# Performance work log

Measured on AMD Instinct MI355X. Metric: run time of the kernel, lower is better.

The kernel has to match this reference:

```python
import jax, jax.numpy as jnp
import numpy as np

N, E, D, H, L = 20000, 320000, 128, 8, 3
C = D // H  # per-head channels = 16


def setup_inputs() -> dict:
    key = jax.random.key(0)
    ks = jax.random.split(key, 20)
    s = 1.0 / np.sqrt(D)
    inp = {
        "x": jax.random.normal(ks[0], (N, D), dtype=jnp.float32),
        "edge_index": jax.random.randint(ks[1], (2, E), 0, N, dtype=jnp.int64),
        "Wq": jax.random.normal(ks[2], (L, D, D), dtype=jnp.float32) * s,
        "bq": jnp.zeros((L, D), dtype=jnp.float32),
        "Wk": jax.random.normal(ks[3], (L, D, D), dtype=jnp.float32) * s,
        "bk": jnp.zeros((L, D), dtype=jnp.float32),
        "Wv": jax.random.normal(ks[4], (L, D, D), dtype=jnp.float32) * s,
        "bv": jnp.zeros((L, D), dtype=jnp.float32),
        "Wskip": jax.random.normal(ks[5], (L, D, D), dtype=jnp.float32) * s,
        "bskip": jnp.zeros((L, D), dtype=jnp.float32),
        "Wbeta": jax.random.normal(ks[6], (L, 3 * D, 1), dtype=jnp.float32) * (1.0 / np.sqrt(3 * D)),
        "ln_g": jnp.ones((L, D), dtype=jnp.float32),
        "ln_b": jnp.zeros((L, D), dtype=jnp.float32),
        "Wout": jax.random.normal(ks[7], (D, D), dtype=jnp.float32) * s,
        "bout": jnp.zeros((D,), dtype=jnp.float32),
    }
    return inp


def _layer_norm(x, g, b, eps=1e-5):
    mu = jnp.mean(x, axis=-1, keepdims=True)
    var = jnp.mean(jnp.square(x - mu), axis=-1, keepdims=True)
    return (x - mu) * jax.lax.rsqrt(var + eps) * g + b


def _transformer_conv(x, src, dst, Wq, bq, Wk, bk, Wv, bv, Wskip, bskip, Wbeta):
    # project q/k/v: [N, D] -> [N, H, C]
    q = (x @ Wq + bq).reshape(N, H, C)
    k = (x @ Wk + bk).reshape(N, H, C)
    v = (x @ Wv + bv).reshape(N, H, C)
    # per-edge attention logits: [E, H]
    alpha = jnp.sum(q[dst] * k[src], axis=-1) / np.sqrt(C)
    # scatter-softmax over edges grouped by dst node
    m = jax.ops.segment_max(alpha, dst, num_segments=N)  # [N, H]
    m = jnp.where(jnp.isfinite(m), m, 0.0)
    ea = jnp.exp(alpha - m[dst])
    denom = jax.ops.segment_sum(ea, dst, num_segments=N)  # [N, H]
    attn = ea / (denom[dst] + 1e-16)  # [E, H]
    # weighted message aggregation: [N, H, C] -> [N, D]
    out = jax.ops.segment_sum(attn[:, :, None] * v[src], dst, num_segments=N)
    out = out.reshape(N, D)
    # beta-gated skip connection (beta=True, root_weight=True)
    x_r = x @ Wskip + bskip
    beta = jax.nn.sigmoid(jnp.concatenate([out, x_r, out - x_r], axis=-1) @ Wbeta)  # [N, 1]
    return beta * x_r + (1.0 - beta) * out


def reference(x, edge_index, Wq, bq, Wk, bk, Wv, bv, Wskip, bskip, Wbeta, ln_g, ln_b, Wout, bout):
    src, dst = edge_index[0], edge_index[1]
    for i in range(L):
        residual = x
        x = _transformer_conv(x, src, dst, Wq[i], bq[i], Wk[i], bk[i], Wv[i], bv[i],
                              Wskip[i], bskip[i], Wbeta[i])
        x = jax.nn.relu(x)  # dropout is identity in eval mode
        x = _layer_norm(x + residual, ln_g[i], ln_b[i])
    return x @ Wout + bout
```

## Files before the change

### kernel.cpp

```cpp
#include <hip/hip_runtime.h>

#define N_NODES 20000
#define N_EDGES 320000
#define DIM 128
#define NLAYER 3
#define SCAN_BLK 1024
#define N_SCAN_BLKS ((N_NODES + SCAN_BLK - 1) / SCAN_BLK)
#define LDS_STRIDE 136

typedef __attribute__((ext_vector_type(8))) short short8;
typedef __attribute__((ext_vector_type(4))) float f32x4;

__device__ inline ushort f2bf(float f) {
  uint u = __float_as_uint(f);
  uint r = (u + 0x7fffu + ((u >> 16) & 1u)) >> 16;
  return (ushort)r;
}
__device__ inline float bf2f(ushort u) { return __uint_as_float(((uint)u) << 16); }


__global__ void zero_ints_kernel(int* __restrict__ p, int n) {
  int i = blockIdx.x * 256 + threadIdx.x;
  if (i < n) p[i] = 0;
}

__global__ void count_deg_kernel(const int* __restrict__ ei, int* __restrict__ deg) {
  int e = blockIdx.x * 256 + threadIdx.x;
  if (e < N_EDGES) atomicAdd(&deg[ei[N_EDGES + e]], 1);
}

__global__ __launch_bounds__(SCAN_BLK) void scan1_kernel(const int* __restrict__ deg,
                                                         int* __restrict__ rowptr,
                                                         int* __restrict__ blksum) {
  __shared__ int wsum[16];
  int t = threadIdx.x, lane = t & 63, w = t >> 6;
  int i = blockIdx.x * SCAN_BLK + t;
  int val = (i < N_NODES) ? deg[i] : 0;
  int s = val;
  #pragma unroll
  for (int off = 1; off < 64; off <<= 1) {
    int u = __shfl_up(s, off);
    if (lane >= off) s += u;
  }
  if (lane == 63) wsum[w] = s;
  __syncthreads();
  if (t < 16) {
    int wv = wsum[t];
    int ss = wv;
    #pragma unroll
    for (int off = 1; off < 16; off <<= 1) {
      int u = __shfl_up(ss, off);
      if (t >= off) ss += u;
    }
    wsum[t] = ss - wv;
  }
  __syncthreads();
  int excl = wsum[w] + s - val;
  if (i < N_NODES) rowptr[i] = excl;
  if (t == SCAN_BLK - 1) blksum[blockIdx.x] = excl + val;
}

__global__ void scan2_kernel(int* __restrict__ blksum, int* __restrict__ rowptr) {
  int t = threadIdx.x;
  int val = (t < N_SCAN_BLKS) ? blksum[t] : 0;
  int s = val;
  #pragma unroll
  for (int off = 1; off < 64; off <<= 1) {
    int u = __shfl_up(s, off);
    if (t >= off) s += u;
  }
  if (t < N_SCAN_BLKS) blksum[t] = s - val;
  if (t == 63) rowptr[N_NODES] = s;
}

__global__ __launch_bounds__(SCAN_BLK) void scan3_kernel(int* __restrict__ rowptr,
                                                         const int* __restrict__ blksum,
                                                         int* __restrict__ degc) {
  int i = blockIdx.x * SCAN_BLK + threadIdx.x;
  if (i < N_NODES) {
    rowptr[i] += blksum[blockIdx.x];
    degc[i] = 0;
  }
}

__global__ void scatter_kernel(const int* __restrict__ ei, const int* __restrict__ rowptr,
                               int* __restrict__ cursor, int* __restrict__ csr_src) {
  int e = blockIdx.x * 256 + threadIdx.x;
  if (e < N_EDGES) {
    int d = ei[N_EDGES + e];
    int s = ei[e];
    int pos = atomicAdd(&cursor[d], 1);
    csr_src[rowptr[d] + pos] = s;
  }
}


__global__ void cast_x_kernel(const float* __restrict__ x, ushort* __restrict__ xb, int n4) {
  int i = blockIdx.x * 256 + threadIdx.x;
  if (i < n4) {
    float4 f = ((const float4*)x)[i];
    ushort4 o;
    o.x = f2bf(f.x); o.y = f2bf(f.y); o.z = f2bf(f.z); o.w = f2bf(f.w);
    ((ushort4*)xb)[i] = o;
  }
}

__global__ void cast_w_kernel(const float* __restrict__ Wq, const float* __restrict__ Wk,
                              const float* __restrict__ Wv, const float* __restrict__ Ws,
                              const float* __restrict__ Wo, ushort* __restrict__ wt) {
  int z = blockIdx.z;
  const float* src;
  if (z < 12) {
    int l = z >> 2, j = z & 3;
    src = (j == 0 ? Wq : j == 1 ? Wk : j == 2 ? Wv : Ws) + (size_t)l * DIM * DIM;
  } else {
    src = Wo;
  }
  __shared__ float tile[32][33];
  int tx = threadIdx.x, ty = threadIdx.y;
  int k0 = blockIdx.x * 32, n0 = blockIdx.y * 32;
  #pragma unroll
  for (int i = 0; i < 32; i += 8)
    tile[ty + i][tx] = src[(size_t)(k0 + ty + i) * DIM + n0 + tx];
  __syncthreads();
  ushort* dst = wt + (size_t)z * DIM * DIM;
  #pragma unroll
  for (int i = 0; i < 32; i += 8)
    dst[(size_t)(n0 + ty + i) * DIM + k0 + tx] = f2bf(tile[tx][ty + i]);
}

template <int OUT_BF16>
__global__ __launch_bounds__(256) void gemm_mfma_kernel(
    const ushort* __restrict__ X, const ushort* __restrict__ WT,
    const float* __restrict__ B0, const float* __restrict__ B1,
    const float* __restrict__ B2, const float* __restrict__ B3,
    void* __restrict__ O0, void* __restrict__ O1, void* __restrict__ O2,
    void* __restrict__ O3) {
  __shared__ ushort As[128 * LDS_STRIDE];
  int mat = blockIdx.y;
  const ushort* Wt = WT + (size_t)mat * DIM * DIM;
  const float* bias;
  void* O;
  switch (mat) {
    case 0: bias = B0; O = O0; break;
    case 1: bias = B1; O = O1; break;
    case 2: bias = B2; O = O2; break;
    default: bias = B3; O = O3; break;
  }
  int t = threadIdx.x;
  int wid = t >> 6, lane = t & 63;
  int row0 = blockIdx.x * 128;
  int wr = wid >> 1, wc = wid & 1;
  int lr = lane & 15;
  int kc8 = (lane >> 4) * 8;

  {
    int rowi = t >> 4;
    int col = (t & 15) * 8;
    #pragma unroll
    for (int pass = 0; pass < 8; ++pass) {
      int row = pass * 16 + rowi;
      int gr = min(row0 + row, N_NODES - 1);
      short8 val = *(const short8*)(X + (size_t)gr * DIM + col);
      *(short8*)(As + row * LDS_STRIDE + col) = val;
    }
  }
  __syncthreads();

  f32x4 acc[4][4];
  #pragma unroll
  for (int i = 0; i < 4; ++i)
    #pragma unroll
    for (int j = 0; j < 4; ++j) acc[i][j] = (f32x4){0.f, 0.f, 0.f, 0.f};

  #pragma unroll
  for (int ks = 0; ks < 4; ++ks) {
    short8 b[4];
    #pragma unroll
    for (int cf = 0; cf < 4; ++cf) {
      int c = wc * 64 + cf * 16 + lr;
      b[cf] = *(const short8*)(Wt + (size_t)c * DIM + ks * 32 + kc8);
    }
    #pragma unroll
    for (int rf = 0; rf < 4; ++rf) {
      int r = wr * 64 + rf * 16 + lr;
      short8 a = *(const short8*)(As + r * LDS_STRIDE + ks * 32 + kc8);
      #pragma unroll
      for (int cf = 0; cf < 4; ++cf)
        acc[rf][cf] = __builtin_amdgcn_mfma_f32_16x16x32_bf16(a, b[cf], acc[rf][cf], 0, 0, 0);
    }
  }

  #pragma unroll
  for (int cf = 0; cf < 4; ++cf) {
    int c = wc * 64 + cf * 16 + lr;
    float bv = bias[c];
    #pragma unroll
    for (int rf = 0; rf < 4; ++rf) {
      #pragma unroll
      for (int reg = 0; reg < 4; ++reg) {
        int r = row0 + wr * 64 + rf * 16 + (lane >> 4) * 4 + reg;
        if (r < N_NODES) {
          float val = acc[rf][cf][reg] + bv;
          if (OUT_BF16)
            ((ushort*)O)[(size_t)r * DIM + c] = f2bf(val);
          else
            ((float*)O)[(size_t)r * DIM + c] = val;
        }
      }
    }
  }
}

__global__ __launch_bounds__(64) void attn_fused_kernel(
    const ushort* __restrict__ q, const ushort* __restrict__ k, const ushort* __restrict__ v,
    const ushort* __restrict__ xr, const float* __restrict__ xres,
    const int* __restrict__ rowptr, const int* __restrict__ csr_src,
    const float* __restrict__ wbeta, const float* __restrict__ lng,
    const float* __restrict__ lnb, float* __restrict__ xnext,
    ushort* __restrict__ xnextb) {
  __shared__ float lds_s[8][20];
  int n = blockIdx.x;
  int lane = threadIdx.x;
  int h = lane & 7, e = lane >> 3;

  const ushort* qrow = q + (size_t)n * DIM + h * 16;
  short8 q0 = *(const short8*)qrow;
  short8 q1 = *(const short8*)(qrow + 8);
  float qf[16];
  #pragma unroll
  for (int i = 0; i < 8; ++i) {
    qf[i] = bf2f((ushort)q0[i]);
    qf[8 + i] = bf2f((ushort)q1[i]);
  }

  int s0 = rowptr[n];
  int deg = rowptr[n + 1] - s0;
  float acc[16];
  #pragma unroll
  for (int i = 0; i < 16; ++i) acc[i] = 0.f;
  float dsum = 0.f;

  for (int base = 0; base < deg; base += 8) {
    int idx = base + e;
    bool valid = idx < deg;
    int src = csr_src[s0 + min(idx, deg - 1)];
    const ushort* kr = k + (size_t)src * DIM + h * 16;
    const ushort* vr = v + (size_t)src * DIM + h * 16;
    short8 ka = *(const short8*)kr;
    short8 kb2 = *(const short8*)(kr + 8);
    short8 va = *(const short8*)vr;
    short8 vb2 = *(const short8*)(vr + 8);
    float p0 = 0.f, p1 = 0.f;
    #pragma unroll
    for (int i = 0; i < 8; ++i) {
      p0 = fmaf(qf[i], bf2f((ushort)ka[i]), p0);
      p1 = fmaf(qf[8 + i], bf2f((ushort)kb2[i]), p1);
    }
    float ea = __expf((p0 + p1) * 0.25f);
    ea = valid ? ea : 0.f;
    dsum += ea;
    #pragma unroll
    for (int i = 0; i < 8; ++i) {
      acc[i] = fmaf(ea, bf2f((ushort)va[i]), acc[i]);
      acc[8 + i] = fmaf(ea, bf2f((ushort)vb2[i]), acc[8 + i]);
    }
  }

  #pragma unroll
  for (int off = 8; off <= 32; off <<= 1) {
    dsum += __shfl_xor(dsum, off);
    #pragma unroll
    for (int i = 0; i < 16; ++i) acc[i] += __shfl_xor(acc[i], off);
  }
  if (lane < 8) {
    #pragma unroll
    for (int i = 0; i < 16; i += 4)
      *(float4*)&lds_s[lane][i] = make_float4(acc[i], acc[i + 1], acc[i + 2], acc[i + 3]);
    lds_s[lane][16] = dsum;
  }
  __syncthreads();

  int c0 = lane * 2;
  int hh = lane >> 3, cc = (lane & 7) * 2;
  float2 ov = *(float2*)&lds_s[hh][cc];
  float den = lds_s[hh][16];
  float inv = 1.f / (den + 1e-16f);
  float o0 = ov.x * inv, o1 = ov.y * inv;

  ushort2 xru = *(const ushort2*)(xr + (size_t)n * DIM + c0);
  float xr0 = bf2f(xru.x), xr1 = bf2f(xru.y);
  float wa0 = wbeta[c0] + wbeta[2 * DIM + c0];
  float wa1 = wbeta[c0 + 1] + wbeta[2 * DIM + c0 + 1];
  float wb0 = wbeta[DIM + c0] - wbeta[2 * DIM + c0];
  float wb1 = wbeta[DIM + c0 + 1] - wbeta[2 * DIM + c0 + 1];
  float bs = o0 * wa0 + o1 * wa1 + xr0 * wb0 + xr1 * wb1;
  #pragma unroll
  for (int off = 1; off < 64; off <<= 1) bs += __shfl_xor(bs, off);
  float beta = 1.f / (1.f + __expf(-bs));
  float y0 = fmaxf(beta * xr0 + (1.f - beta) * o0, 0.f);
  float y1 = fmaxf(beta * xr1 + (1.f - beta) * o1, 0.f);
  float2 rv = *(const float2*)(xres + (size_t)n * DIM + c0);
  y0 += rv.x;
  y1 += rv.y;
  float s = y0 + y1;
  #pragma unroll
  for (int off = 1; off < 64; off <<= 1) s += __shfl_xor(s, off);
  float mu = s * (1.f / 128.f);
  float d0 = y0 - mu, d1 = y1 - mu;
  float vs = d0 * d0 + d1 * d1;
  #pragma unroll
  for (int off = 1; off < 64; off <<= 1) vs += __shfl_xor(vs, off);
  float rstd = rsqrtf(vs * (1.f / 128.f) + 1e-5f);
  float2 g = *(const float2*)(lng + c0);
  float2 b = *(const float2*)(lnb + c0);
  float out0 = d0 * rstd * g.x + b.x;
  float out1 = d1 * rstd * g.y + b.y;
  *(float2*)(xnext + (size_t)n * DIM + c0) = make_float2(out0, out1);
  ushort2 ob;
  ob.x = f2bf(out0);
  ob.y = f2bf(out1);
  *(ushort2*)(xnextb + (size_t)n * DIM + c0) = ob;
}


extern "C" void kernel_launch(void* const* d_in, const int* in_sizes, int n_in,
                              void* d_out, int out_size, void* d_ws, size_t ws_size,
                              hipStream_t stream) {
  const float* x_in = (const float*)d_in[0];
  const int* ei = (const int*)d_in[1];
  const float* Wq = (const float*)d_in[2];
  const float* bq = (const float*)d_in[3];
  const float* Wk = (const float*)d_in[4];
  const float* bk = (const float*)d_in[5];
  const float* Wv = (const float*)d_in[6];
  const float* bv = (const float*)d_in[7];
  const float* Wsk = (const float*)d_in[8];
  const float* bsk = (const float*)d_in[9];
  const float* Wb = (const float*)d_in[10];
  const float* lng = (const float*)d_in[11];
  const float* lnb = (const float*)d_in[12];
  const float* Wout = (const float*)d_in[13];
  const float* bout = (const float*)d_in[14];
  float* out = (float*)d_out;

  char* p = (char*)d_ws;
  auto alloc = [&](size_t bytes) {
    char* r = p;
    p += (bytes + 255) & ~(size_t)255;
    return r;
  };
  const size_t NB2 = (size_t)N_NODES * DIM * 2;
  const size_t NB4 = (size_t)N_NODES * DIM * 4;
  ushort* xbb = (ushort*)alloc(NB2);
  ushort* qb = (ushort*)alloc(NB2);
  ushort* kb = (ushort*)alloc(NB2);
  ushort* vb = (ushort*)alloc(NB2);
  ushort* xrb = (ushort*)alloc(NB2);
  float* xf0 = (float*)alloc(NB4);
  float* xf1 = (float*)alloc(NB4);
  ushort* wt = (ushort*)alloc((size_t)13 * DIM * DIM * 2);
  int* rowptr = (int*)alloc((N_NODES + 1) * 4);
  int* degc = (int*)alloc(N_NODES * 4);
  int* blksum = (int*)alloc(64 * 4);
  int* csr_src = (int*)alloc(N_EDGES * 4);

  zero_ints_kernel<<<(N_NODES + 255) / 256, 256, 0, stream>>>(degc, N_NODES);
  count_deg_kernel<<<(N_EDGES + 255) / 256, 256, 0, stream>>>(ei, degc);
  scan1_kernel<<<N_SCAN_BLKS, SCAN_BLK, 0, stream>>>(degc, rowptr, blksum);
  scan2_kernel<<<1, 64, 0, stream>>>(blksum, rowptr);
  scan3_kernel<<<N_SCAN_BLKS, SCAN_BLK, 0, stream>>>(rowptr, blksum, degc);
  scatter_kernel<<<(N_EDGES + 255) / 256, 256, 0, stream>>>(ei, rowptr, degc, csr_src);

  cast_x_kernel<<<(N_NODES * DIM / 4 + 255) / 256, 256, 0, stream>>>(x_in, xbb,
                                                                     N_NODES * DIM / 4);
  cast_w_kernel<<<dim3(4, 4, 13), dim3(32, 8), 0, stream>>>(Wq, Wk, Wv, Wsk, Wout, wt);

  const int GX = (N_NODES + 127) / 128;
  const float* xres = x_in;
  float* xfbufs[NLAYER] = {xf0, xf1, xf0};
  for (int l = 0; l < NLAYER; ++l) {
    gemm_mfma_kernel<1><<<dim3(GX, 4), 256, 0, stream>>>(
        xbb, wt + (size_t)l * 4 * DIM * DIM,
        bq + (size_t)l * DIM, bk + (size_t)l * DIM, bv + (size_t)l * DIM,
        bsk + (size_t)l * DIM, qb, kb, vb, xrb);
    attn_fused_kernel<<<N_NODES, 64, 0, stream>>>(
        qb, kb, vb, xrb, xres, rowptr, csr_src,
        Wb + (size_t)l * 3 * DIM, lng + (size_t)l * DIM, lnb + (size_t)l * DIM,
        xfbufs[l], xbb);
    xres = xfbufs[l];
  }
  gemm_mfma_kernel<0><<<dim3(GX, 1), 256, 0, stream>>>(
      xbb, wt + (size_t)12 * DIM * DIM, bout, bout, bout, bout, out, out, out, out);
}
```

Measured before the change: 218.1 us.

## Interleave K/V rows, pack 4 nodes per attention block, merge prep kernels

K and V projections are written into one interleaved buffer with a 256-element row stride, so each gathered source node's K and V sit in a single contiguous 512-byte row instead of two separate arrays. The attention kernel now processes four destination nodes per 256-thread block rather than one node per 64-thread block, reducing block count and scheduling overhead. The x cast, weight transpose-cast and degree zeroing are merged into one prep kernel to cut launch count. The GEMM gains per-output strides to support the interleaved layout.

```diff
diff --git a/kernel.cpp b/kernel.cpp
--- a/kernel.cpp
+++ b/kernel.cpp
@@ -8,6 +8,11 @@
 #define N_SCAN_BLKS ((N_NODES + SCAN_BLK - 1) / SCAN_BLK)
 #define LDS_STRIDE 136
 
+#define PREP_CASTX_BLKS 2500
+#define PREP_CASTW_BLKS 208
+#define PREP_ZERO_BLKS 79
+#define PREP_TOTAL (PREP_CASTX_BLKS + PREP_CASTW_BLKS + PREP_ZERO_BLKS)
+
 typedef __attribute__((ext_vector_type(8))) short short8;
 typedef __attribute__((ext_vector_type(4))) float f32x4;
 
@@ -18,11 +23,48 @@
 }
 __device__ inline float bf2f(ushort u) { return __uint_as_float(((uint)u) << 16); }
 
-
-__global__ void zero_ints_kernel(int* __restrict__ p, int n) {
-  int i = blockIdx.x * 256 + threadIdx.x;
-  if (i < n) p[i] = 0;
-}
+__global__ __launch_bounds__(256) void prep_kernel(
+    const float* __restrict__ x, ushort* __restrict__ xb,
+    const float* __restrict__ Wq, const float* __restrict__ Wk,
+    const float* __restrict__ Wv, const float* __restrict__ Ws,
+    const float* __restrict__ Wo, ushort* __restrict__ wt,
+    int* __restrict__ degc) {
+  int b = blockIdx.x;
+  int t = threadIdx.x;
+  if (b < PREP_CASTX_BLKS) {
+    int i = b * 256 + t;
+    float4 f = ((const float4*)x)[i];
+    ushort4 o;
+    o.x = f2bf(f.x); o.y = f2bf(f.y); o.z = f2bf(f.z); o.w = f2bf(f.w);
+    ((ushort4*)xb)[i] = o;
+  } else if (b < PREP_CASTX_BLKS + PREP_CASTW_BLKS) {
+    int idx = b - PREP_CASTX_BLKS;
+    int z = idx >> 4;
+    int r = idx & 15;
+    int k0 = (r >> 2) * 32, n0 = (r & 3) * 32;
+    const float* src;
+    if (z < 12) {
+      int l = z >> 2, j = z & 3;
+      src = (j == 0 ? Wq : j == 1 ? Wk : j == 2 ? Wv : Ws) + (size_t)l * DIM * DIM;
+    } else {
+      src = Wo;
+    }
+    __shared__ float tile[32][33];
+    int tx = t & 31, ty = t >> 5;
+    #pragma unroll
+    for (int i = 0; i < 32; i += 8)
+      tile[ty + i][tx] = src[(size_t)(k0 + ty + i) * DIM + n0 + tx];
+    __syncthreads();
+    ushort* dst = wt + (size_t)z * DIM * DIM;
+    #pragma unroll
+    for (int i = 0; i < 32; i += 8)
+      dst[(size_t)(n0 + ty + i) * DIM + k0 + tx] = f2bf(tile[tx][ty + i]);
+  } else {
+    int i = (b - PREP_CASTX_BLKS - PREP_CASTW_BLKS) * 256 + t;
+    if (i < N_NODES) degc[i] = 0;
+  }
+}
+
 
 __global__ void count_deg_kernel(const int* __restrict__ ei, int* __restrict__ deg) {
   int e = blockIdx.x * 256 + threadIdx.x;
@@ -94,58 +136,24 @@
   }
 }
 
-
-__global__ void cast_x_kernel(const float* __restrict__ x, ushort* __restrict__ xb, int n4) {
-  int i = blockIdx.x * 256 + threadIdx.x;
-  if (i < n4) {
-    float4 f = ((const float4*)x)[i];
-    ushort4 o;
-    o.x = f2bf(f.x); o.y = f2bf(f.y); o.z = f2bf(f.z); o.w = f2bf(f.w);
-    ((ushort4*)xb)[i] = o;
-  }
-}
-
-__global__ void cast_w_kernel(const float* __restrict__ Wq, const float* __restrict__ Wk,
-                              const float* __restrict__ Wv, const float* __restrict__ Ws,
-                              const float* __restrict__ Wo, ushort* __restrict__ wt) {
-  int z = blockIdx.z;
-  const float* src;
-  if (z < 12) {
-    int l = z >> 2, j = z & 3;
-    src = (j == 0 ? Wq : j == 1 ? Wk : j == 2 ? Wv : Ws) + (size_t)l * DIM * DIM;
-  } else {
-    src = Wo;
-  }
-  __shared__ float tile[32][33];
-  int tx = threadIdx.x, ty = threadIdx.y;
-  int k0 = blockIdx.x * 32, n0 = blockIdx.y * 32;
-  #pragma unroll
-  for (int i = 0; i < 32; i += 8)
-    tile[ty + i][tx] = src[(size_t)(k0 + ty + i) * DIM + n0 + tx];
-  __syncthreads();
-  ushort* dst = wt + (size_t)z * DIM * DIM;
-  #pragma unroll
-  for (int i = 0; i < 32; i += 8)
-    dst[(size_t)(n0 + ty + i) * DIM + k0 + tx] = f2bf(tile[tx][ty + i]);
-}
-
 template <int OUT_BF16>
 __global__ __launch_bounds__(256) void gemm_mfma_kernel(
     const ushort* __restrict__ X, const ushort* __restrict__ WT,
     const float* __restrict__ B0, const float* __restrict__ B1,
     const float* __restrict__ B2, const float* __restrict__ B3,
     void* __restrict__ O0, void* __restrict__ O1, void* __restrict__ O2,
-    void* __restrict__ O3) {
+    void* __restrict__ O3, int st0, int st1, int st2, int st3) {
   __shared__ ushort As[128 * LDS_STRIDE];
   int mat = blockIdx.y;
   const ushort* Wt = WT + (size_t)mat * DIM * DIM;
   const float* bias;
   void* O;
+  int ost;
   switch (mat) {
-    case 0: bias = B0; O = O0; break;
-    case 1: bias = B1; O = O1; break;
-    case 2: bias = B2; O = O2; break;
-    default: bias = B3; O = O3; break;
+    case 0: bias = B0; O = O0; ost = st0; break;
+    case 1: bias = B1; O = O1; ost = st1; break;
+    case 2: bias = B2; O = O2; ost = st2; break;
+    default: bias = B3; O = O3; ost = st3; break;
   }
   int t = threadIdx.x;
   int wid = t >> 6, lane = t & 63;
@@ -203,25 +211,26 @@
         if (r < N_NODES) {
           float val = acc[rf][cf][reg] + bv;
           if (OUT_BF16)
-            ((ushort*)O)[(size_t)r * DIM + c] = f2bf(val);
+            ((ushort*)O)[(size_t)r * ost + c] = f2bf(val);
           else
-            ((float*)O)[(size_t)r * DIM + c] = val;
+            ((float*)O)[(size_t)r * ost + c] = val;
         }
       }
     }
   }
 }
 
-__global__ __launch_bounds__(64) void attn_fused_kernel(
-    const ushort* __restrict__ q, const ushort* __restrict__ k, const ushort* __restrict__ v,
+__global__ __launch_bounds__(256) void attn_fused_kernel(
+    const ushort* __restrict__ q, const ushort* __restrict__ kv,
     const ushort* __restrict__ xr, const float* __restrict__ xres,
     const int* __restrict__ rowptr, const int* __restrict__ csr_src,
     const float* __restrict__ wbeta, const float* __restrict__ lng,
     const float* __restrict__ lnb, float* __restrict__ xnext,
     ushort* __restrict__ xnextb) {
-  __shared__ float lds_s[8][20];
-  int n = blockIdx.x;
-  int lane = threadIdx.x;
+  __shared__ float lds_s[4][8][20];
+  int w = threadIdx.x >> 6;
+  int lane = threadIdx.x & 63;
+  int n = blockIdx.x * 4 + w;
   int h = lane & 7, e = lane >> 3;
 
   const ushort* qrow = q + (size_t)n * DIM + h * 16;
@@ -245,12 +254,11 @@
     int idx = base + e;
     bool valid = idx < deg;
     int src = csr_src[s0 + min(idx, deg - 1)];
-    const ushort* kr = k + (size_t)src * DIM + h * 16;
-    const ushort* vr = v + (size_t)src * DIM + h * 16;
+    const ushort* kr = kv + (size_t)src * 256 + h * 16;
     short8 ka = *(const short8*)kr;
     short8 kb2 = *(const short8*)(kr + 8);
-    short8 va = *(const short8*)vr;
-    short8 vb2 = *(const short8*)(vr + 8);
+    short8 va = *(const short8*)(kr + 128);
+    short8 vb2 = *(const short8*)(kr + 136);
     float p0 = 0.f, p1 = 0.f;
     #pragma unroll
     for (int i = 0; i < 8; ++i) {
@@ -276,15 +284,15 @@
   if (lane < 8) {
     #pragma unroll
     for (int i = 0; i < 16; i += 4)
-      *(float4*)&lds_s[lane][i] = make_float4(acc[i], acc[i + 1], acc[i + 2], acc[i + 3]);
-    lds_s[lane][16] = dsum;
+      *(float4*)&lds_s[w][lane][i] = make_float4(acc[i], acc[i + 1], acc[i + 2], acc[i + 3]);
+    lds_s[w][lane][16] = dsum;
   }
   __syncthreads();
 
   int c0 = lane * 2;
   int hh = lane >> 3, cc = (lane & 7) * 2;
-  float2 ov = *(float2*)&lds_s[hh][cc];
-  float den = lds_s[hh][16];
+  float2 ov = *(float2*)&lds_s[w][hh][cc];
+  float den = lds_s[w][hh][16];
   float inv = 1.f / (den + 1e-16f);
   float o0 = ov.x * inv, o1 = ov.y * inv;
 
@@ -354,8 +362,7 @@
   const size_t NB4 = (size_t)N_NODES * DIM * 4;
   ushort* xbb = (ushort*)alloc(NB2);
   ushort* qb = (ushort*)alloc(NB2);
-  ushort* kb = (ushort*)alloc(NB2);
-  ushort* vb = (ushort*)alloc(NB2);
+  ushort* kvb = (ushort*)alloc(NB2 * 2);
   ushort* xrb = (ushort*)alloc(NB2);
   float* xf0 = (float*)alloc(NB4);
   float* xf1 = (float*)alloc(NB4);
@@ -365,16 +372,13 @@
   int* blksum = (int*)alloc(64 * 4);
   int* csr_src = (int*)alloc(N_EDGES * 4);
 
-  zero_ints_kernel<<<(N_NODES + 255) / 256, 256, 0, stream>>>(degc, N_NODES);
+  prep_kernel<<<PREP_TOTAL, 256, 0, stream>>>(x_in, xbb, Wq, Wk, Wv, Wsk, Wout, wt, degc);
+
   count_deg_kernel<<<(N_EDGES + 255) / 256, 256, 0, stream>>>(ei, degc);
   scan1_kernel<<<N_SCAN_BLKS, SCAN_BLK, 0, stream>>>(degc, rowptr, blksum);
   scan2_kernel<<<1, 64, 0, stream>>>(blksum, rowptr);
   scan3_kernel<<<N_SCAN_BLKS, SCAN_BLK, 0, stream>>>(rowptr, blksum, degc);
   scatter_kernel<<<(N_EDGES + 255) / 256, 256, 0, stream>>>(ei, rowptr, degc, csr_src);
-
-  cast_x_kernel<<<(N_NODES * DIM / 4 + 255) / 256, 256, 0, stream>>>(x_in, xbb,
-                                                                     N_NODES * DIM / 4);
-  cast_w_kernel<<<dim3(4, 4, 13), dim3(32, 8), 0, stream>>>(Wq, Wk, Wv, Wsk, Wout, wt);
 
   const int GX = (N_NODES + 127) / 128;
   const float* xres = x_in;
@@ -383,13 +387,15 @@
     gemm_mfma_kernel<1><<<dim3(GX, 4), 256, 0, stream>>>(
         xbb, wt + (size_t)l * 4 * DIM * DIM,
         bq + (size_t)l * DIM, bk + (size_t)l * DIM, bv + (size_t)l * DIM,
-        bsk + (size_t)l * DIM, qb, kb, vb, xrb);
-    attn_fused_kernel<<<N_NODES, 64, 0, stream>>>(
-        qb, kb, vb, xrb, xres, rowptr, csr_src,
+        bsk + (size_t)l * DIM,
+        qb, kvb, kvb + 128, xrb, DIM, 256, 256, DIM);
+    attn_fused_kernel<<<N_NODES / 4, 256, 0, stream>>>(
+        qb, kvb, xrb, xres, rowptr, csr_src,
         Wb + (size_t)l * 3 * DIM, lng + (size_t)l * DIM, lnb + (size_t)l * DIM,
         xfbufs[l], xbb);
     xres = xfbufs[l];
   }
   gemm_mfma_kernel<0><<<dim3(GX, 1), 256, 0, stream>>>(
-      xbb, wt + (size_t)12 * DIM * DIM, bout, bout, bout, bout, out, out, out, out);
-}
+      xbb, wt + (size_t)12 * DIM * DIM, bout, bout, bout, bout,
+      out, out, out, out, DIM, DIM, DIM, DIM);
+}
```

Measured after the change: 217.7 us. Within noise of the previous version (-0.2%).
